# Performance work log

Hardware: AMD Instinct MI355X
Metric: run time of the kernel (lower is better)

The kernel has to match this reference:

```python
import jax, jax.numpy as jnp
import numpy as np

NUM_STATES = 16
INPUT_DIM = 1024
QUANTUM_DIM = 1024
LN_EPS = 1e-5


def setup_inputs() -> dict:
    key = jax.random.key(0)
    ks = jax.random.split(key, 7)
    # stacked per-state Linear weights: [S, input_dim, quantum_dim]
    W = jax.random.normal(ks[0], (NUM_STATES, INPUT_DIM, QUANTUM_DIM), jnp.float32) * (1.0 / np.sqrt(INPUT_DIM))
    b = jax.random.normal(ks[1], (NUM_STATES, QUANTUM_DIM), jnp.float32) * 0.01
    amplitude_weights = jax.random.normal(ks[2], (NUM_STATES, QUANTUM_DIM), jnp.float32)
    phase_weights = jax.random.normal(ks[3], (NUM_STATES, QUANTUM_DIM), jnp.float32)
    ln_gamma = jnp.ones((QUANTUM_DIM,), jnp.float32)
    ln_beta = jnp.zeros((QUANTUM_DIM,), jnp.float32)
    language_features = jax.random.normal(ks[4], (4096, INPUT_DIM), jnp.float32)
    return {
        "language_features": language_features,
        "W": W,
        "b": b,
        "amplitude_weights": amplitude_weights,
        "phase_weights": phase_weights,
        "ln_gamma": ln_gamma,
        "ln_beta": ln_beta,
    }


def reference(language_features, W, b, amplitude_weights, phase_weights, ln_gamma, ln_beta):
    # Per-state linear projections as one batched GEMM: [B, S, Q]
    states = jnp.einsum("bi,siq->bsq", language_features, W) + b[None, :, :]
    # amplitudes = softmax over states (dim=0 in torch)
    amplitudes = jax.nn.softmax(amplitude_weights, axis=0)  # [S, Q]
    # real(amplitude * exp(i*phase) * state) = amplitude * cos(phase) * state
    mix = amplitudes * jnp.cos(phase_weights)  # [S, Q]
    sup = states * mix[None, :, :]  # [B, S, Q]
    # LayerNorm over last dim
    mean = jnp.mean(sup, axis=-1, keepdims=True)
    var = jnp.var(sup, axis=-1, keepdims=True)
    out = (sup - mean) * jax.lax.rsqrt(var + LN_EPS) * ln_gamma + ln_beta
    return out
```

## Files before the change

### kernel.cpp

```cpp
#include <hip/hip_runtime.h>

typedef __attribute__((ext_vector_type(8))) short short8;
typedef __attribute__((ext_vector_type(4))) float f32x4;
typedef __attribute__((ext_vector_type(4))) unsigned short u16x4;

#define GLOAD16(g, l)                                                          \
  __builtin_amdgcn_global_load_lds(                                            \
      (const __attribute__((address_space(1))) unsigned int*)(g),              \
      (__attribute__((address_space(3))) unsigned int*)(l), 16, 0, 0)

__device__ __forceinline__ unsigned short f2bf(float f) {
  unsigned int u = __float_as_uint(f);
  u += 0x7FFFu + ((u >> 16) & 1u);
  return (unsigned short)(u >> 16);
}
__device__ __forceinline__ float bf2f(unsigned short h) {
  return __uint_as_float(((unsigned int)h) << 16);
}

__global__ void mix_kernel(const float* __restrict__ amp,
                           const float* __restrict__ phase,
                           const float* __restrict__ bias,
                           float* __restrict__ mix, float* __restrict__ bmix) {
  int q = blockIdx.x * blockDim.x + threadIdx.x;
  float a[16];
  float mx = -1e30f;
  for (int s = 0; s < 16; ++s) {
    a[s] = amp[s * 1024 + q];
    mx = fmaxf(mx, a[s]);
  }
  float sum = 0.f;
  for (int s = 0; s < 16; ++s) {
    a[s] = __expf(a[s] - mx);
    sum += a[s];
  }
  float inv = 1.f / sum;
  for (int s = 0; s < 16; ++s) {
    float m = a[s] * inv * cosf(phase[s * 1024 + q]);
    mix[s * 1024 + q] = m;
    bmix[s * 1024 + q] = bias[s * 1024 + q] * m;
  }
}

__global__ void cast_x_kernel(const float* __restrict__ x,
                              unsigned short* __restrict__ xb) {
  int i = (blockIdx.x * blockDim.x + threadIdx.x) * 4;
  float4 v = *(const float4*)(x + i);
  union { unsigned short h[4]; uint2 u; } o;
  o.h[0] = f2bf(v.x); o.h[1] = f2bf(v.y); o.h[2] = f2bf(v.z); o.h[3] = f2bf(v.w);
  *(uint2*)(xb + i) = o.u;
}

__global__ __launch_bounds__(256) void transpose_w_kernel(
    const float* __restrict__ W, const float* __restrict__ mix,
    unsigned short* __restrict__ Wt) {
  __shared__ unsigned short tile[64][66];
  const int s = blockIdx.z;
  const int q0 = blockIdx.x * 64, i0 = blockIdx.y * 64;
  const int t = threadIdx.x;
  const float* Ws = W + (size_t)s * 1048576;
  unsigned short* Wts = Wt + (size_t)s * 1048576;
  const int rq = t & 63, ri = t >> 6;
  const float mv = mix[s * 1024 + q0 + rq];
  #pragma unroll
  for (int p = 0; p < 16; ++p)
    tile[p * 4 + ri][rq] =
        f2bf(Ws[(size_t)(i0 + p * 4 + ri) * 1024 + q0 + rq] * mv);
  __syncthreads();
  const int wq = t >> 3, wi = (t & 7) * 8;
  #pragma unroll
  for (int o = 0; o < 2; ++o) {
    union { unsigned short h[8]; short8 v; } u;
    #pragma unroll
    for (int e = 0; e < 8; ++e) u.h[e] = tile[wi + e][o * 32 + wq];
    *(short8*)(Wts + (size_t)(q0 + o * 32 + wq) * 1024 + i0 + wi) = u.v;
  }
}

template <bool BF16SUP>
__global__ __launch_bounds__(256) void gemm_kernel(
    const unsigned short* __restrict__ xb, const unsigned short* __restrict__ wt,
    const float* __restrict__ bmix,
    float* __restrict__ outf, unsigned short* __restrict__ sup) {
  __shared__ __align__(16) unsigned short Abuf[3][128 * 32];
  __shared__ __align__(16) unsigned short Bbuf[3][128 * 32];

  const int tid = threadIdx.x;
  const int lane = tid & 63;
  const int wv = tid >> 6;
  const int wm = wv >> 1, wn = wv & 1;
  const int m0 = blockIdx.y * 128;
  const int n0 = blockIdx.x * 128;

  const int c0 = tid, c1 = tid + 256;
  const int r0 = c0 >> 2, k80 = (c0 & 3) * 8;
  const int r1 = c1 >> 2, k81 = (c1 & 3) * 8;
  const unsigned short* ga0 = xb + (size_t)(m0 + r0) * 1024 + k80;
  const unsigned short* ga1 = xb + (size_t)(m0 + r1) * 1024 + k81;
  const unsigned short* gb0 = wt + (size_t)(n0 + r0) * 1024 + k80;
  const unsigned short* gb1 = wt + (size_t)(n0 + r1) * 1024 + k81;

#define STAGE(kt, b) do {                                                      \
    const int _ko = (kt) * 32;                                                 \
    GLOAD16(ga0 + _ko, &Abuf[b][c0 * 8]);                                      \
    GLOAD16(ga1 + _ko, &Abuf[b][c1 * 8]);                                      \
    GLOAD16(gb0 + _ko, &Bbuf[b][c0 * 8]);                                      \
    GLOAD16(gb1 + _ko, &Bbuf[b][c1 * 8]);                                      \
  } while (0)

  f32x4 acc[4][4];
  #pragma unroll
  for (int i = 0; i < 4; ++i)
    #pragma unroll
    for (int j = 0; j < 4; ++j) acc[i][j] = (f32x4){0.f, 0.f, 0.f, 0.f};

  STAGE(0, 0);
  STAGE(1, 1);
  asm volatile("s_waitcnt vmcnt(4)" ::: "memory");
  __builtin_amdgcn_s_barrier();

  const int lr = lane & 15;
  const int lk = (lane >> 4) * 8;
  int cur = 0;
  for (int kt = 0; kt < 32; ++kt) {
    if (kt < 30) {
      int nb = cur + 2; if (nb >= 3) nb -= 3;
      STAGE(kt + 2, nb);
    }
    short8 af[4], bfr[4];
    #pragma unroll
    for (int mi = 0; mi < 4; ++mi)
      af[mi] = *(const short8*)&Abuf[cur][(wm * 64 + mi * 16 + lr) * 32 + lk];
    #pragma unroll
    for (int ni = 0; ni < 4; ++ni)
      bfr[ni] = *(const short8*)&Bbuf[cur][(wn * 64 + ni * 16 + lr) * 32 + lk];
    asm volatile("s_waitcnt lgkmcnt(0)" ::: "memory");
    if (kt < 30) {
      asm volatile("s_waitcnt vmcnt(4)" ::: "memory");
    } else if (kt == 30) {
      asm volatile("s_waitcnt vmcnt(0)" ::: "memory");
    }
    __builtin_amdgcn_sched_barrier(0);
    __builtin_amdgcn_s_barrier();
    #pragma unroll
    for (int mi = 0; mi < 4; ++mi)
      #pragma unroll
      for (int ni = 0; ni < 4; ++ni)
        acc[mi][ni] = __builtin_amdgcn_mfma_f32_16x16x32_bf16(
            af[mi], bfr[ni], acc[mi][ni], 0, 0, 0);
    cur += 1; if (cur >= 3) cur = 0;
  }
#undef STAGE

  #pragma unroll
  for (int ni = 0; ni < 4; ++ni) {
    const int n = n0 + wn * 64 + ni * 16 + lr;
    const float bv = bmix[n];
    #pragma unroll
    for (int mi = 0; mi < 4; ++mi) {
      const int m = m0 + wm * 64 + mi * 16 + (lane >> 4) * 4;
      #pragma unroll
      for (int r = 0; r < 4; ++r) {
        float v = acc[mi][ni][r] + bv;
        if (BF16SUP)
          sup[(size_t)(m + r) * 16384 + n] = f2bf(v);
        else
          outf[(size_t)(m + r) * 16384 + n] = v;
      }
    }
  }
}

__global__ __launch_bounds__(256) void ln_bf16_kernel(
    const unsigned short* __restrict__ sup, float* __restrict__ out,
    const float* __restrict__ gamma, const float* __restrict__ beta) {
  __shared__ float red[8];
  const int t = threadIdx.x;
  const size_t base = (size_t)blockIdx.x * 1024;
  u16x4 raw = *(const u16x4*)(sup + base + t * 4);
  float v[4];
  #pragma unroll
  for (int j = 0; j < 4; ++j) v[j] = bf2f(raw[j]);
  float s = v[0] + v[1] + v[2] + v[3];
  float ss = v[0] * v[0] + v[1] * v[1] + v[2] * v[2] + v[3] * v[3];
  #pragma unroll
  for (int m = 32; m >= 1; m >>= 1) {
    s += __shfl_xor(s, m);
    ss += __shfl_xor(ss, m);
  }
  const int wv = t >> 6;
  if ((t & 63) == 0) { red[wv * 2] = s; red[wv * 2 + 1] = ss; }
  __syncthreads();
  const float S = red[0] + red[2] + red[4] + red[6];
  const float SS = red[1] + red[3] + red[5] + red[7];
  const float mean = S * (1.0f / 1024.0f);
  const float var = SS * (1.0f / 1024.0f) - mean * mean;
  const float rstd = rsqrtf(var + 1e-5f);
  const float4 g = *(const float4*)(gamma + t * 4);
  const float4 b = *(const float4*)(beta + t * 4);
  float4 o;
  o.x = (v[0] - mean) * rstd * g.x + b.x;
  o.y = (v[1] - mean) * rstd * g.y + b.y;
  o.z = (v[2] - mean) * rstd * g.z + b.z;
  o.w = (v[3] - mean) * rstd * g.w + b.w;
  *(float4*)(out + base + t * 4) = o;
}

__global__ __launch_bounds__(256) void ln_kernel(float* __restrict__ out,
                                                 const float* __restrict__ gamma,
                                                 const float* __restrict__ beta) {
  __shared__ float red[8];
  const int t = threadIdx.x;
  const size_t base = (size_t)blockIdx.x * 1024;
  float4 v = *(const float4*)(out + base + t * 4);
  float s = v.x + v.y + v.z + v.w;
  float ss = v.x * v.x + v.y * v.y + v.z * v.z + v.w * v.w;
  #pragma unroll
  for (int m = 32; m >= 1; m >>= 1) {
    s += __shfl_xor(s, m);
    ss += __shfl_xor(ss, m);
  }
  const int wv = t >> 6;
  if ((t & 63) == 0) { red[wv * 2] = s; red[wv * 2 + 1] = ss; }
  __syncthreads();
  const float S = red[0] + red[2] + red[4] + red[6];
  const float SS = red[1] + red[3] + red[5] + red[7];
  const float mean = S * (1.0f / 1024.0f);
  const float var = SS * (1.0f / 1024.0f) - mean * mean;
  const float rstd = rsqrtf(var + 1e-5f);
  const float4 g = *(const float4*)(gamma + t * 4);
  const float4 b = *(const float4*)(beta + t * 4);
  float4 o;
  o.x = (v.x - mean) * rstd * g.x + b.x;
  o.y = (v.y - mean) * rstd * g.y + b.y;
  o.z = (v.z - mean) * rstd * g.z + b.z;
  o.w = (v.w - mean) * rstd * g.w + b.w;
  *(float4*)(out + base + t * 4) = o;
}

extern "C" void kernel_launch(void* const* d_in, const int* in_sizes, int n_in,
                              void* d_out, int out_size, void* d_ws, size_t ws_size,
                              hipStream_t stream) {
  (void)in_sizes; (void)n_in; (void)out_size;
  const float* x     = (const float*)d_in[0];
  const float* W     = (const float*)d_in[1];
  const float* bias  = (const float*)d_in[2];
  const float* amp   = (const float*)d_in[3];
  const float* phase = (const float*)d_in[4];
  const float* gamma = (const float*)d_in[5];
  const float* beta  = (const float*)d_in[6];
  float* out = (float*)d_out;

  const bool big = ws_size >= (size_t)134217728ULL;

  unsigned short *Wt, *xbuf, *supb = nullptr;
  float *mixp, *bmixp;
  if (big) {
    char* ob = (char*)d_out;
    Wt    = (unsigned short*)ob;
    xbuf  = (unsigned short*)(ob + 33554432);
    mixp  = (float*)(ob + 41943040);
    bmixp = mixp + 16384;
    supb  = (unsigned short*)d_ws;
  } else {
    char* ws = (char*)d_ws;
    Wt    = (unsigned short*)ws;
    xbuf  = (unsigned short*)(ws + 33554432);
    mixp  = (float*)(ws + 33554432 + 8388608);
    bmixp = mixp + 16384;
  }

  hipLaunchKernelGGL(mix_kernel, dim3(4), dim3(256), 0, stream, amp, phase, bias, mixp, bmixp);
  hipLaunchKernelGGL(cast_x_kernel, dim3(4096), dim3(256), 0, stream, x, xbuf);
  hipLaunchKernelGGL(transpose_w_kernel, dim3(16, 16, 16), dim3(256), 0, stream, W, mixp, Wt);
  if (big) {
    hipLaunchKernelGGL((gemm_kernel<true>), dim3(128, 32), dim3(256), 0, stream,
                       xbuf, Wt, bmixp, out, supb);
    hipLaunchKernelGGL(ln_bf16_kernel, dim3(65536), dim3(256), 0, stream,
                       supb, out, gamma, beta);
  } else {
    hipLaunchKernelGGL((gemm_kernel<false>), dim3(128, 32), dim3(256), 0, stream,
                       xbuf, Wt, bmixp, out, nullptr);
    hipLaunchKernelGGL(ln_kernel, dim3(65536), dim3(256), 0, stream, out, gamma, beta);
  }
}
```

Before: 300.0 us.

## Double-buffer LDS fragment reads in GEMM and vectorize weight transpose

The GEMM main loop is restructured to prefetch the next k-tile's LDS fragments into a second register set while the current set's MFMAs run, overlapping LDS reads with matrix math. The loop is manually unrolled by two with ping-pong register buffers. Separately, the weight transpose kernel now uses float4 global loads, packed bf16 LDS writes, a different padding, and one 32-byte store per thread. This raises register pressure in the GEMM and changes the LDS bank pattern in the transpose.

```diff
diff --git a/kernel.cpp b/kernel.cpp
--- a/kernel.cpp
+++ b/kernel.cpp
@@ -54,27 +54,38 @@
 __global__ __launch_bounds__(256) void transpose_w_kernel(
     const float* __restrict__ W, const float* __restrict__ mix,
     unsigned short* __restrict__ Wt) {
-  __shared__ unsigned short tile[64][66];
+  __shared__ unsigned short tile[64][68];
   const int s = blockIdx.z;
   const int q0 = blockIdx.x * 64, i0 = blockIdx.y * 64;
   const int t = threadIdx.x;
   const float* Ws = W + (size_t)s * 1048576;
   unsigned short* Wts = Wt + (size_t)s * 1048576;
-  const int rq = t & 63, ri = t >> 6;
-  const float mv = mix[s * 1024 + q0 + rq];
-  #pragma unroll
-  for (int p = 0; p < 16; ++p)
-    tile[p * 4 + ri][rq] =
-        f2bf(Ws[(size_t)(i0 + p * 4 + ri) * 1024 + q0 + rq] * mv);
+  const int rq = (t & 15) * 4;
+  const int ri = t >> 4;
+  const float4 mv = *(const float4*)(mix + s * 1024 + q0 + rq);
+  #pragma unroll
+  for (int p = 0; p < 4; ++p) {
+    const int i = p * 16 + ri;
+    float4 v = *(const float4*)(Ws + (size_t)(i0 + i) * 1024 + q0 + rq);
+    union { unsigned short h[4]; uint2 u; } pk;
+    pk.h[0] = f2bf(v.x * mv.x);
+    pk.h[1] = f2bf(v.y * mv.y);
+    pk.h[2] = f2bf(v.z * mv.z);
+    pk.h[3] = f2bf(v.w * mv.w);
+    *(uint2*)&tile[i][rq] = pk.u;
+  }
   __syncthreads();
-  const int wq = t >> 3, wi = (t & 7) * 8;
-  #pragma unroll
-  for (int o = 0; o < 2; ++o) {
-    union { unsigned short h[8]; short8 v; } u;
-    #pragma unroll
-    for (int e = 0; e < 8; ++e) u.h[e] = tile[wi + e][o * 32 + wq];
-    *(short8*)(Wts + (size_t)(q0 + o * 32 + wq) * 1024 + i0 + wi) = u.v;
-  }
+  const int wq = t >> 2;
+  const int wi = (t & 3) * 16;
+  union { unsigned short h[8]; short8 v8; } u0, u1;
+  #pragma unroll
+  for (int e = 0; e < 8; ++e) {
+    u0.h[e] = tile[wi + e][wq];
+    u1.h[e] = tile[wi + 8 + e][wq];
+  }
+  unsigned short* dst = Wts + (size_t)(q0 + wq) * 1024 + i0 + wi;
+  *(short8*)dst = u0.v8;
+  *(short8*)(dst + 8) = u1.v8;
 }
 
 template <bool BF16SUP>
@@ -114,43 +125,66 @@
     #pragma unroll
     for (int j = 0; j < 4; ++j) acc[i][j] = (f32x4){0.f, 0.f, 0.f, 0.f};
 
+  const int lr = lane & 15;
+  const int lk = (lane >> 4) * 8;
+
+#define READS(AF, BF, b) do {                                                  \
+    const unsigned short* _ab = &Abuf[b][(wm * 64 + lr) * 32 + lk];            \
+    _Pragma("unroll")                                                          \
+    for (int mi = 0; mi < 4; ++mi)                                             \
+      AF[mi] = *(const short8*)(_ab + mi * 16 * 32);                           \
+    const unsigned short* _bb = &Bbuf[b][(wn * 64 + lr) * 32 + lk];            \
+    _Pragma("unroll")                                                          \
+    for (int ni = 0; ni < 4; ++ni)                                             \
+      BF[ni] = *(const short8*)(_bb + ni * 16 * 32);                           \
+  } while (0)
+
+#define MFMASET(AF, BF)                                                        \
+    _Pragma("unroll")                                                          \
+    for (int mi = 0; mi < 4; ++mi)                                             \
+      _Pragma("unroll")                                                        \
+      for (int ni = 0; ni < 4; ++ni)                                           \
+        acc[mi][ni] = __builtin_amdgcn_mfma_f32_16x16x32_bf16(                 \
+            AF[mi], BF[ni], acc[mi][ni], 0, 0, 0)
+
+#define LGKM0() do { asm volatile("s_waitcnt lgkmcnt(0)" ::: "memory");        \
+                     __builtin_amdgcn_sched_barrier(0); } while (0)
+
+  short8 afA[4], bfA[4], afB[4], bfB[4];
+
   STAGE(0, 0);
   STAGE(1, 1);
   asm volatile("s_waitcnt vmcnt(4)" ::: "memory");
   __builtin_amdgcn_s_barrier();
-
-  const int lr = lane & 15;
-  const int lk = (lane >> 4) * 8;
-  int cur = 0;
-  for (int kt = 0; kt < 32; ++kt) {
-    if (kt < 30) {
-      int nb = cur + 2; if (nb >= 3) nb -= 3;
-      STAGE(kt + 2, nb);
-    }
-    short8 af[4], bfr[4];
-    #pragma unroll
-    for (int mi = 0; mi < 4; ++mi)
-      af[mi] = *(const short8*)&Abuf[cur][(wm * 64 + mi * 16 + lr) * 32 + lk];
-    #pragma unroll
-    for (int ni = 0; ni < 4; ++ni)
-      bfr[ni] = *(const short8*)&Bbuf[cur][(wn * 64 + ni * 16 + lr) * 32 + lk];
-    asm volatile("s_waitcnt lgkmcnt(0)" ::: "memory");
-    if (kt < 30) {
-      asm volatile("s_waitcnt vmcnt(4)" ::: "memory");
-    } else if (kt == 30) {
-      asm volatile("s_waitcnt vmcnt(0)" ::: "memory");
-    }
+  READS(afA, bfA, 0);
+
+  int b0 = 0;
+  #pragma unroll 1
+  for (int it = 0; it < 16; ++it) {
+    const int kt0 = 2 * it, kt1 = kt0 + 1;
+    int b1 = b0 + 1; if (b1 >= 3) b1 -= 3;
+    int b2 = b0 + 2; if (b2 >= 3) b2 -= 3;
+    if (kt0 < 30) STAGE(kt0 + 2, b2);
+    LGKM0();
+    if (kt0 < 30) asm volatile("s_waitcnt vmcnt(4)" ::: "memory");
+    else          asm volatile("s_waitcnt vmcnt(0)" ::: "memory");
     __builtin_amdgcn_sched_barrier(0);
     __builtin_amdgcn_s_barrier();
-    #pragma unroll
-    for (int mi = 0; mi < 4; ++mi)
-      #pragma unroll
-      for (int ni = 0; ni < 4; ++ni)
-        acc[mi][ni] = __builtin_amdgcn_mfma_f32_16x16x32_bf16(
-            af[mi], bfr[ni], acc[mi][ni], 0, 0, 0);
-    cur += 1; if (cur >= 3) cur = 0;
+    READS(afB, bfB, b1);
+    MFMASET(afA, bfA);
+    if (kt1 < 30) STAGE(kt1 + 2, b0);
+    LGKM0();
+    if (kt1 < 30) asm volatile("s_waitcnt vmcnt(4)" ::: "memory");
+    __builtin_amdgcn_sched_barrier(0);
+    __builtin_amdgcn_s_barrier();
+    if (kt1 < 31) READS(afA, bfA, b2);
+    MFMASET(afB, bfB);
+    b0 = b2;
   }
 #undef STAGE
+#undef READS
+#undef MFMASET
+#undef LGKM0
 
   #pragma unroll
   for (int ni = 0; ni < 4; ++ni) {
```

Result: no change. 299.6 us (-0.1%).
